# Kernel tuning notes

Hardware: AMD Instinct MI355X
Metric: run time of the kernel (lower is better)

The kernel has to match this reference:

```python
import jax, jax.numpy as jnp
import numpy as np

B, S, D, H = 16, 8192, 512, 512
NEG_INF = -1e18


def setup_inputs() -> dict:
    key0 = jax.random.key(0)
    ks = jax.random.split(key0, 8)
    scale = 1.0 / np.sqrt(D)
    return {
        "query": jax.random.normal(ks[0], (B, D), dtype=jnp.float32),
        "key": jax.random.normal(ks[1], (B, S, D), dtype=jnp.float32),
        "mask": jax.random.bernoulli(ks[2], 0.1, (B, S)),
        # q_proj: Linear(D -> H) with bias
        "Wq": jax.random.uniform(ks[3], (H, D), jnp.float32, -scale, scale),
        "bq": jax.random.uniform(ks[4], (H,), jnp.float32, -scale, scale),
        # k_proj: Conv1d(D -> H, kernel=1) == pointwise Linear with bias
        "Wk": jax.random.uniform(ks[5], (H, D), jnp.float32, -scale, scale),
        "bk": jax.random.uniform(ks[6], (H,), jnp.float32, -scale, scale),
        # out_proj: Linear(H -> 1, bias=False), init uniform(-1, 1)
        "w_out": jax.random.uniform(ks[7], (H,), jnp.float32, -1.0, 1.0),
    }


def reference(query, key, mask, Wq, bq, Wk, bk, w_out):
    # q_proj: (B, D) -> (B, H)
    q_h = query @ Wq.T + bq
    # k_proj (1x1 conv): (B, S, D) -> (B, S, H)
    k_h = jnp.einsum("bsd,hd->bsh", key, Wk) + bk
    # score = w_out . (q_h broadcast + k_h)  -> (B, S)
    attn_weight = jnp.einsum("bsh,h->bs", q_h[:, None, :] + k_h, w_out)
    attn_weight = jnp.where(mask, NEG_INF, attn_weight)
    attn_prob = jax.nn.softmax(attn_weight, axis=-1)
    # weighted sum over projected keys: (B, H)
    attn = jnp.einsum("bsh,bs->bh", k_h, attn_prob)
    return attn, attn_weight
```

## Files before the change

kernel.cpp:

```cpp
#include <hip/hip_runtime.h>
#include <math.h>

#define BB 16
#define SS 8192
#define DD 512
#define HH 512
#define NEG_INF (-1e18f)
#define BPB 64

__device__ __forceinline__ float dot8(float4 a0, float4 a1, float4 b0, float4 b1) {
  return a0.x*b0.x + a0.y*b0.y + a0.z*b0.z + a0.w*b0.w
       + a1.x*b1.x + a1.y*b1.y + a1.z*b1.z + a1.w*b1.w;
}

template <int CTRL>
__device__ __forceinline__ float dpp_add0(float x) {
  return x + __int_as_float(__builtin_amdgcn_update_dpp(
      0, __float_as_int(x), CTRL, 0xf, 0xf, true));
}
__device__ __forceinline__ float wave_red_sum(float x) {
  x = dpp_add0<0x111>(x);
  x = dpp_add0<0x112>(x);
  x = dpp_add0<0x114>(x);
  x = dpp_add0<0x118>(x);
  x = dpp_add0<0x142>(x);
  x = dpp_add0<0x143>(x);
  return x;
}
__device__ __forceinline__ float lane63(float x) {
  return __int_as_float(__builtin_amdgcn_readlane(__float_as_int(x), 63));
}
template <int CTRL>
__device__ __forceinline__ float dpp_maxstep(float x) {
  int y = __builtin_amdgcn_update_dpp(
      __float_as_int(x), __float_as_int(x), CTRL, 0xf, 0xf, false);
  return fmaxf(x, __int_as_float(y));
}
__device__ __forceinline__ float wave_red_max(float x) {
  x = dpp_maxstep<0x111>(x); x = dpp_maxstep<0x112>(x);
  x = dpp_maxstep<0x114>(x); x = dpp_maxstep<0x118>(x);
  x = dpp_maxstep<0x142>(x); x = dpp_maxstep<0x143>(x);
  return x;
}

__global__ __launch_bounds__(256) void k_prep(
    const float* __restrict__ Wq, const float* __restrict__ Wk,
    const float* __restrict__ wout, const float* __restrict__ bq,
    const float* __restrict__ bk, float* __restrict__ v,
    float* __restrict__ w2, float* __restrict__ c0)
{
  int blk = blockIdx.x;
  int t = threadIdx.x;
  if (blk == 128) {
    if (t < 64) {
      float part = 0.f;
      #pragma unroll
      for (int i = 0; i < 8; ++i) {
        int h = t + 64 * i;
        part += wout[h] * (bq[h] + bk[h]);
      }
      part = wave_red_sum(part);
      if (t == 63) c0[0] = part;
    }
    return;
  }
  int j = blk & 63;
  const float* W = (blk < 64) ? Wk : Wq;
  float* outp = (blk < 64) ? v : w2;
  int dsl = j * 8;
  int h0 = t, h1 = t + 256;
  const float4* r0 = (const float4*)(W + (size_t)h0 * DD + dsl);
  const float4* r1 = (const float4*)(W + (size_t)h1 * DD + dsl);
  float4 a0 = r0[0], a1 = r0[1], b0 = r1[0], b1 = r1[1];
  float wA = wout[h0], wB = wout[h1];
  float acc[8];
  acc[0] = wA*a0.x + wB*b0.x; acc[1] = wA*a0.y + wB*b0.y;
  acc[2] = wA*a0.z + wB*b0.z; acc[3] = wA*a0.w + wB*b0.w;
  acc[4] = wA*a1.x + wB*b1.x; acc[5] = wA*a1.y + wB*b1.y;
  acc[6] = wA*a1.z + wB*b1.z; acc[7] = wA*a1.w + wB*b1.w;
  __shared__ float red[256][9];
  #pragma unroll
  for (int k = 0; k < 8; ++k) red[t][k] = acc[k];
  __syncthreads();
  for (int st = 128; st; st >>= 1) {
    if (t < st) {
      #pragma unroll
      for (int k = 0; k < 8; ++k) red[t][k] += red[t + st][k];
    }
    __syncthreads();
  }
  if (t < 8) outp[dsl + t] = red[0][t];
}

__global__ __launch_bounds__(256, 4) void k_score(
    const float* __restrict__ key, const int* __restrict__ mask,
    const float* __restrict__ query, const float* __restrict__ ws_v,
    const float* __restrict__ ws_w2, const float* __restrict__ ws_c0,
    float* __restrict__ scores, float* __restrict__ partials)
{
  int blk = blockIdx.x;
  int b = blk / BPB;
  int pb = blk % BPB;
  const int rows = SS / BPB;
  int s0 = pb * rows;
  int wave = threadIdx.x >> 6;
  int lane = threadIdx.x & 63;

  const float4* vv = (const float4*)ws_v;
  float4 v0 = vv[lane], v1 = vv[64 + lane];

  float qc;
  {
    const float4* q4 = (const float4*)(query + (size_t)b * DD);
    const float4* w24 = (const float4*)ws_w2;
    float qp = wave_red_sum(dot8(q4[lane], q4[64 + lane], w24[lane], w24[64 + lane]));
    qc = lane63(qp) + ws_c0[0];
  }

  const float4* keyb = (const float4*)(key + (size_t)b * SS * DD);
  const int* maskb = mask + b * SS;

  float m = -INFINITY, l = 0.f;
  float4 u0 = {0.f,0.f,0.f,0.f}, u1 = {0.f,0.f,0.f,0.f};

  const int nit = rows / 16;
  int s = s0 + wave * 4;

  float4 r0a, r0b, r1a, r1b, r2a, r2b, r3a, r3b;
  {
    const float4* p0 = keyb + (size_t)s * (DD / 4);
    r0a = p0[lane];       r0b = p0[64 + lane];
    r1a = p0[128 + lane]; r1b = p0[192 + lane];
    r2a = p0[256 + lane]; r2b = p0[320 + lane];
    r3a = p0[384 + lane]; r3b = p0[448 + lane];
  }
  int4 mk = *(const int4*)(maskb + s);

  for (int i = 0; i < nit; ++i) {
    float4 n0a=r0a, n0b=r0b, n1a=r1a, n1b=r1b, n2a=r2a, n2b=r2b, n3a=r3a, n3b=r3b;
    int4 nmk = {0,0,0,0};
    if (i + 1 < nit) {
      const float4* p0 = keyb + (size_t)(s + 16) * (DD / 4);
      n0a = p0[lane];       n0b = p0[64 + lane];
      n1a = p0[128 + lane]; n1b = p0[192 + lane];
      n2a = p0[256 + lane]; n2b = p0[320 + lane];
      n3a = p0[384 + lane]; n3b = p0[448 + lane];
      nmk = *(const int4*)(maskb + s + 16);
    }
    float p0v = wave_red_sum(dot8(r0a, r0b, v0, v1));
    float p1v = wave_red_sum(dot8(r1a, r1b, v0, v1));
    float p2v = wave_red_sum(dot8(r2a, r2b, v0, v1));
    float p3v = wave_red_sum(dot8(r3a, r3b, v0, v1));
    float d0 = lane63(p0v), d1 = lane63(p1v);
    float d2 = lane63(p2v), d3 = lane63(p3v);
    float sc0 = mk.x ? NEG_INF : (d0 + qc);
    float sc1 = mk.y ? NEG_INF : (d1 + qc);
    float sc2 = mk.z ? NEG_INF : (d2 + qc);
    float sc3 = mk.w ? NEG_INF : (d3 + qc);
    if (lane == 0) {
      float4 st = {sc0, sc1, sc2, sc3};
      *(float4*)(scores + (size_t)b * SS + s) = st;
    }
    float mn = fmaxf(fmaxf(fmaxf(sc0, sc1), fmaxf(sc2, sc3)), m);
    if (mn > m) {
      float sc = __expf(m - mn);
      l *= sc;
      u0.x *= sc; u0.y *= sc; u0.z *= sc; u0.w *= sc;
      u1.x *= sc; u1.y *= sc; u1.z *= sc; u1.w *= sc;
      m = mn;
    }
    float e0 = __expf(sc0 - m), e1 = __expf(sc1 - m);
    float e2 = __expf(sc2 - m), e3 = __expf(sc3 - m);
    l += (e0 + e1) + (e2 + e3);
    u0.x += e0*r0a.x + e1*r1a.x + e2*r2a.x + e3*r3a.x;
    u0.y += e0*r0a.y + e1*r1a.y + e2*r2a.y + e3*r3a.y;
    u0.z += e0*r0a.z + e1*r1a.z + e2*r2a.z + e3*r3a.z;
    u0.w += e0*r0a.w + e1*r1a.w + e2*r2a.w + e3*r3a.w;
    u1.x += e0*r0b.x + e1*r1b.x + e2*r2b.x + e3*r3b.x;
    u1.y += e0*r0b.y + e1*r1b.y + e2*r2b.y + e3*r3b.y;
    u1.z += e0*r0b.z + e1*r1b.z + e2*r2b.z + e3*r3b.z;
    u1.w += e0*r0b.w + e1*r1b.w + e2*r2b.w + e3*r3b.w;
    r0a=n0a; r0b=n0b; r1a=n1a; r1b=n1b; r2a=n2a; r2b=n2b; r3a=n3a; r3b=n3b;
    mk = nmk; s += 16;
  }

  __shared__ float ls_m[4], ls_l[4];
  __shared__ __align__(16) float ls_u[4][DD];
  ls_u[wave][4 * lane + 0] = u0.x; ls_u[wave][4 * lane + 1] = u0.y;
  ls_u[wave][4 * lane + 2] = u0.z; ls_u[wave][4 * lane + 3] = u0.w;
  ls_u[wave][256 + 4 * lane + 0] = u1.x; ls_u[wave][256 + 4 * lane + 1] = u1.y;
  ls_u[wave][256 + 4 * lane + 2] = u1.z; ls_u[wave][256 + 4 * lane + 3] = u1.w;
  if (lane == 0) { ls_m[wave] = m; ls_l[wave] = l; }
  __syncthreads();

  float M = fmaxf(fmaxf(ls_m[0], ls_m[1]), fmaxf(ls_m[2], ls_m[3]));
  float f0 = __expf(ls_m[0] - M), f1 = __expf(ls_m[1] - M);
  float f2 = __expf(ls_m[2] - M), f3 = __expf(ls_m[3] - M);
  int d = threadIdx.x;
  float ua = ls_u[0][d] * f0 + ls_u[1][d] * f1 + ls_u[2][d] * f2 + ls_u[3][d] * f3;
  float ub = ls_u[0][d + 256] * f0 + ls_u[1][d + 256] * f1
           + ls_u[2][d + 256] * f2 + ls_u[3][d + 256] * f3;
  float* part = partials + (size_t)(b * BPB + pb) * (DD + 2);
  part[2 + d] = ua;
  part[2 + 256 + d] = ub;
  if (threadIdx.x == 0) {
    part[0] = M;
    part[1] = ls_l[0] * f0 + ls_l[1] * f1 + ls_l[2] * f2 + ls_l[3] * f3;
  }
}

__global__ __launch_bounds__(256) void k_out(
    const float* __restrict__ Wk, const float* __restrict__ bk,
    const float* __restrict__ partials, float* __restrict__ attn)
{
  int b = blockIdx.x >> 4;
  int hc = blockIdx.x & 15;
  int tid = threadIdx.x;
  int wave = tid >> 6, lane = tid & 63;
  __shared__ __align__(16) float ubar[DD];
  __shared__ float fsh[BPB];
  __shared__ float dsh;
  const float* pbase = partials + (size_t)b * BPB * (DD + 2);

  if (tid < 64) {
    float mp = pbase[tid * (DD + 2)];
    float lp = pbase[tid * (DD + 2) + 1];
    float M = lane63(wave_red_max(mp));
    float f = __expf(mp - M);
    fsh[tid] = f;
    float dn = wave_red_sum(lp * f);
    if (tid == 63) dsh = dn;
  }
  __syncthreads();

  float inv = 1.f / dsh;
  float ua = 0.f, ub_ = 0.f;
  #pragma unroll 8
  for (int p = 0; p < BPB; ++p) {
    float f = fsh[p];
    ua  += pbase[p * (DD + 2) + 2 + tid] * f;
    ub_ += pbase[p * (DD + 2) + 2 + 256 + tid] * f;
  }
  ubar[tid] = ua * inv;
  ubar[tid + 256] = ub_ * inv;
  __syncthreads();

  const float4* ub4 = (const float4*)ubar;
  float4 x0 = ub4[lane], x1 = ub4[64 + lane];
  #pragma unroll
  for (int j = 0; j < 8; ++j) {
    int h = hc * 32 + wave * 8 + j;
    const float4* wr = (const float4*)(Wk + (size_t)h * DD);
    float p = wave_red_sum(dot8(wr[lane], wr[64 + lane], x0, x1));
    if (lane == 63) attn[b * HH + h] = p + bk[h];
  }
}

extern "C" void kernel_launch(void* const* d_in, const int* in_sizes, int n_in,
                              void* d_out, int out_size, void* d_ws, size_t ws_size,
                              hipStream_t stream) {
  const float* query = (const float*)d_in[0];
  const float* key   = (const float*)d_in[1];
  const int*   mask  = (const int*)d_in[2];
  const float* Wq    = (const float*)d_in[3];
  const float* bq    = (const float*)d_in[4];
  const float* Wk    = (const float*)d_in[5];
  const float* bk    = (const float*)d_in[6];
  const float* wout  = (const float*)d_in[7];

  float* out    = (float*)d_out;
  float* attn   = out;
  float* scores = out + BB * HH;
  float* ws     = (float*)d_ws;

  float* ws_v  = ws;
  float* ws_w2 = ws + 512;
  float* ws_c0 = ws + 1024;
  float* partials = ws + 1040;

  k_prep<<<dim3(129), dim3(256), 0, stream>>>(Wq, Wk, wout, bq, bk,
                                              ws_v, ws_w2, ws_c0);
  k_score<<<dim3(BB * BPB), dim3(256), 0, stream>>>(key, mask, query, ws_v,
                                                    ws_w2, ws_c0, scores, partials);
  k_out<<<dim3(BB * 16), dim3(256), 0, stream>>>(Wk, bk, partials, attn);
}
```

Before: 60.97 us.

## Fuse output reduction into score kernel via last-block atomic counter

```diff
diff --git a/kernel.cpp b/kernel.cpp
--- a/kernel.cpp
+++ b/kernel.cpp
@@ -47,11 +47,13 @@
     const float* __restrict__ Wq, const float* __restrict__ Wk,
     const float* __restrict__ wout, const float* __restrict__ bq,
     const float* __restrict__ bk, float* __restrict__ v,
-    float* __restrict__ w2, float* __restrict__ c0)
+    float* __restrict__ w2, float* __restrict__ c0,
+    unsigned* __restrict__ cnt)
 {
   int blk = blockIdx.x;
   int t = threadIdx.x;
   if (blk == 128) {
+    if (t < BB) cnt[t] = 0u;
     if (t < 64) {
       float part = 0.f;
       #pragma unroll
@@ -96,7 +98,9 @@
     const float* __restrict__ key, const int* __restrict__ mask,
     const float* __restrict__ query, const float* __restrict__ ws_v,
     const float* __restrict__ ws_w2, const float* __restrict__ ws_c0,
-    float* __restrict__ scores, float* __restrict__ partials)
+    const float* __restrict__ Wk, const float* __restrict__ bk,
+    float* __restrict__ scores, float* __restrict__ partials,
+    unsigned* __restrict__ cnt, float* __restrict__ attn)
 {
   int blk = blockIdx.x;
   int b = blk / BPB;
@@ -105,6 +109,10 @@
   int s0 = pb * rows;
   int wave = threadIdx.x >> 6;
   int lane = threadIdx.x & 63;
+
+  __shared__ __align__(16) float smem[4 * DD];
+  __shared__ float ls_m[4], ls_l[4], dsh;
+  __shared__ unsigned sh_old;
 
   const float4* vv = (const float4*)ws_v;
   float4 v0 = vv[lane], v1 = vv[64 + lane];
@@ -184,12 +192,10 @@
     mk = nmk; s += 16;
   }
 
-  __shared__ float ls_m[4], ls_l[4];
-  __shared__ __align__(16) float ls_u[4][DD];
-  ls_u[wave][4 * lane + 0] = u0.x; ls_u[wave][4 * lane + 1] = u0.y;
-  ls_u[wave][4 * lane + 2] = u0.z; ls_u[wave][4 * lane + 3] = u0.w;
-  ls_u[wave][256 + 4 * lane + 0] = u1.x; ls_u[wave][256 + 4 * lane + 1] = u1.y;
-  ls_u[wave][256 + 4 * lane + 2] = u1.z; ls_u[wave][256 + 4 * lane + 3] = u1.w;
+  smem[wave * DD + 4 * lane + 0] = u0.x; smem[wave * DD + 4 * lane + 1] = u0.y;
+  smem[wave * DD + 4 * lane + 2] = u0.z; smem[wave * DD + 4 * lane + 3] = u0.w;
+  smem[wave * DD + 256 + 4 * lane + 0] = u1.x; smem[wave * DD + 256 + 4 * lane + 1] = u1.y;
+  smem[wave * DD + 256 + 4 * lane + 2] = u1.z; smem[wave * DD + 256 + 4 * lane + 3] = u1.w;
   if (lane == 0) { ls_m[wave] = m; ls_l[wave] = l; }
   __syncthreads();
 
@@ -197,9 +203,10 @@
   float f0 = __expf(ls_m[0] - M), f1 = __expf(ls_m[1] - M);
   float f2 = __expf(ls_m[2] - M), f3 = __expf(ls_m[3] - M);
   int d = threadIdx.x;
-  float ua = ls_u[0][d] * f0 + ls_u[1][d] * f1 + ls_u[2][d] * f2 + ls_u[3][d] * f3;
-  float ub = ls_u[0][d + 256] * f0 + ls_u[1][d + 256] * f1
-           + ls_u[2][d + 256] * f2 + ls_u[3][d + 256] * f3;
+  float ua = smem[d] * f0 + smem[DD + d] * f1
+           + smem[2 * DD + d] * f2 + smem[3 * DD + d] * f3;
+  float ub = smem[d + 256] * f0 + smem[DD + d + 256] * f1
+           + smem[2 * DD + d + 256] * f2 + smem[3 * DD + d + 256] * f3;
   float* part = partials + (size_t)(b * BPB + pb) * (DD + 2);
   part[2 + d] = ua;
   part[2 + 256 + d] = ub;
@@ -207,26 +214,26 @@
     part[0] = M;
     part[1] = ls_l[0] * f0 + ls_l[1] * f1 + ls_l[2] * f2 + ls_l[3] * f3;
   }
-}
-
-__global__ __launch_bounds__(256) void k_out(
-    const float* __restrict__ Wk, const float* __restrict__ bk,
-    const float* __restrict__ partials, float* __restrict__ attn)
-{
-  int b = blockIdx.x >> 4;
-  int hc = blockIdx.x & 15;
+
+  __syncthreads();
+  if (threadIdx.x == 0) {
+    __threadfence();
+    sh_old = atomicAdd(&cnt[b], 1u);
+  }
+  __syncthreads();
+  if (sh_old != BPB - 1) return;
+
+  __threadfence();
+  float* ubar = smem;
+  float* fsh  = smem + DD;
+  const float* pbase = partials + (size_t)b * BPB * (DD + 2);
   int tid = threadIdx.x;
-  int wave = tid >> 6, lane = tid & 63;
-  __shared__ __align__(16) float ubar[DD];
-  __shared__ float fsh[BPB];
-  __shared__ float dsh;
-  const float* pbase = partials + (size_t)b * BPB * (DD + 2);
 
   if (tid < 64) {
     float mp = pbase[tid * (DD + 2)];
     float lp = pbase[tid * (DD + 2) + 1];
-    float M = lane63(wave_red_max(mp));
-    float f = __expf(mp - M);
+    float Mx = lane63(wave_red_max(mp));
+    float f = __expf(mp - Mx);
     fsh[tid] = f;
     float dn = wave_red_sum(lp * f);
     if (tid == 63) dsh = dn;
@@ -234,22 +241,22 @@
   __syncthreads();
 
   float inv = 1.f / dsh;
-  float ua = 0.f, ub_ = 0.f;
+  float sa = 0.f, sb = 0.f;
   #pragma unroll 8
   for (int p = 0; p < BPB; ++p) {
     float f = fsh[p];
-    ua  += pbase[p * (DD + 2) + 2 + tid] * f;
-    ub_ += pbase[p * (DD + 2) + 2 + 256 + tid] * f;
-  }
-  ubar[tid] = ua * inv;
-  ubar[tid + 256] = ub_ * inv;
+    sa += pbase[p * (DD + 2) + 2 + tid] * f;
+    sb += pbase[p * (DD + 2) + 2 + 256 + tid] * f;
+  }
+  ubar[tid] = sa * inv;
+  ubar[tid + 256] = sb * inv;
   __syncthreads();
 
   const float4* ub4 = (const float4*)ubar;
   float4 x0 = ub4[lane], x1 = ub4[64 + lane];
-  #pragma unroll
-  for (int j = 0; j < 8; ++j) {
-    int h = hc * 32 + wave * 8 + j;
+  #pragma unroll 4
+  for (int j = 0; j < 128; ++j) {
+    int h = wave * 128 + j;
     const float4* wr = (const float4*)(Wk + (size_t)h * DD);
     float p = wave_red_sum(dot8(wr[lane], wr[64 + lane], x0, x1));
     if (lane == 63) attn[b * HH + h] = p + bk[h];
@@ -276,11 +283,12 @@
   float* ws_v  = ws;
   float* ws_w2 = ws + 512;
   float* ws_c0 = ws + 1024;
-  float* partials = ws + 1040;
+  unsigned* cnt = (unsigned*)(ws + 1040);
+  float* partials = ws + 1056;
 
   k_prep<<<dim3(129), dim3(256), 0, stream>>>(Wq, Wk, wout, bq, bk,
-                                              ws_v, ws_w2, ws_c0);
+                                              ws_v, ws_w2, ws_c0, cnt);
   k_score<<<dim3(BB * BPB), dim3(256), 0, stream>>>(key, mask, query, ws_v,
-                                                    ws_w2, ws_c0, scores, partials);
-  k_out<<<dim3(BB * 16), dim3(256), 0, stream>>>(Wk, bk, partials, attn);
-}
+                                                    ws_w2, ws_c0, Wk, bk,
+                                                    scores, partials, cnt, attn);
+}
```

Result: slower. 162.8 us (+167.1%).

## Template split count, use 128 blocks per batch with 2 rows per wave

Applied to the files above, without the earlier changes.

```diff
diff --git a/kernel.cpp b/kernel.cpp
--- a/kernel.cpp
+++ b/kernel.cpp
@@ -6,7 +6,6 @@
 #define DD 512
 #define HH 512
 #define NEG_INF (-1e18f)
-#define BPB 64
 
 __device__ __forceinline__ float dot8(float4 a0, float4 a1, float4 b0, float4 b1) {
   return a0.x*b0.x + a0.y*b0.y + a0.z*b0.z + a0.w*b0.w
@@ -92,16 +91,17 @@
   if (t < 8) outp[dsl + t] = red[0][t];
 }
 
-__global__ __launch_bounds__(256, 4) void k_score(
+template <int NPB>
+__global__ __launch_bounds__(256, 6) void k_score(
     const float* __restrict__ key, const int* __restrict__ mask,
     const float* __restrict__ query, const float* __restrict__ ws_v,
     const float* __restrict__ ws_w2, const float* __restrict__ ws_c0,
     float* __restrict__ scores, float* __restrict__ partials)
 {
   int blk = blockIdx.x;
-  int b = blk / BPB;
-  int pb = blk % BPB;
-  const int rows = SS / BPB;
+  int b = blk / NPB;
+  int pb = blk % NPB;
+  const int rows = SS / NPB;
   int s0 = pb * rows;
   int wave = threadIdx.x >> 6;
   int lane = threadIdx.x & 63;
@@ -123,45 +123,36 @@
   float m = -INFINITY, l = 0.f;
   float4 u0 = {0.f,0.f,0.f,0.f}, u1 = {0.f,0.f,0.f,0.f};
 
-  const int nit = rows / 16;
-  int s = s0 + wave * 4;
-
-  float4 r0a, r0b, r1a, r1b, r2a, r2b, r3a, r3b;
+  const int nit = rows / 8;
+  int s = s0 + wave * 2;
+
+  float4 r0a, r0b, r1a, r1b;
   {
     const float4* p0 = keyb + (size_t)s * (DD / 4);
     r0a = p0[lane];       r0b = p0[64 + lane];
     r1a = p0[128 + lane]; r1b = p0[192 + lane];
-    r2a = p0[256 + lane]; r2b = p0[320 + lane];
-    r3a = p0[384 + lane]; r3b = p0[448 + lane];
-  }
-  int4 mk = *(const int4*)(maskb + s);
+  }
+  int2 mk = *(const int2*)(maskb + s);
 
   for (int i = 0; i < nit; ++i) {
-    float4 n0a=r0a, n0b=r0b, n1a=r1a, n1b=r1b, n2a=r2a, n2b=r2b, n3a=r3a, n3b=r3b;
-    int4 nmk = {0,0,0,0};
+    float4 n0a=r0a, n0b=r0b, n1a=r1a, n1b=r1b;
+    int2 nmk = {0,0};
     if (i + 1 < nit) {
-      const float4* p0 = keyb + (size_t)(s + 16) * (DD / 4);
+      const float4* p0 = keyb + (size_t)(s + 8) * (DD / 4);
       n0a = p0[lane];       n0b = p0[64 + lane];
       n1a = p0[128 + lane]; n1b = p0[192 + lane];
-      n2a = p0[256 + lane]; n2b = p0[320 + lane];
-      n3a = p0[384 + lane]; n3b = p0[448 + lane];
-      nmk = *(const int4*)(maskb + s + 16);
+      nmk = *(const int2*)(maskb + s + 8);
     }
     float p0v = wave_red_sum(dot8(r0a, r0b, v0, v1));
     float p1v = wave_red_sum(dot8(r1a, r1b, v0, v1));
-    float p2v = wave_red_sum(dot8(r2a, r2b, v0, v1));
-    float p3v = wave_red_sum(dot8(r3a, r3b, v0, v1));
     float d0 = lane63(p0v), d1 = lane63(p1v);
-    float d2 = lane63(p2v), d3 = lane63(p3v);
     float sc0 = mk.x ? NEG_INF : (d0 + qc);
     float sc1 = mk.y ? NEG_INF : (d1 + qc);
-    float sc2 = mk.z ? NEG_INF : (d2 + qc);
-    float sc3 = mk.w ? NEG_INF : (d3 + qc);
     if (lane == 0) {
-      float4 st = {sc0, sc1, sc2, sc3};
-      *(float4*)(scores + (size_t)b * SS + s) = st;
-    }
-    float mn = fmaxf(fmaxf(fmaxf(sc0, sc1), fmaxf(sc2, sc3)), m);
+      float2 st = {sc0, sc1};
+      *(float2*)(scores + (size_t)b * SS + s) = st;
+    }
+    float mn = fmaxf(fmaxf(sc0, sc1), m);
     if (mn > m) {
       float sc = __expf(m - mn);
       l *= sc;
@@ -170,18 +161,13 @@
       m = mn;
     }
     float e0 = __expf(sc0 - m), e1 = __expf(sc1 - m);
-    float e2 = __expf(sc2 - m), e3 = __expf(sc3 - m);
-    l += (e0 + e1) + (e2 + e3);
-    u0.x += e0*r0a.x + e1*r1a.x + e2*r2a.x + e3*r3a.x;
-    u0.y += e0*r0a.y + e1*r1a.y + e2*r2a.y + e3*r3a.y;
-    u0.z += e0*r0a.z + e1*r1a.z + e2*r2a.z + e3*r3a.z;
-    u0.w += e0*r0a.w + e1*r1a.w + e2*r2a.w + e3*r3a.w;
-    u1.x += e0*r0b.x + e1*r1b.x + e2*r2b.x + e3*r3b.x;
-    u1.y += e0*r0b.y + e1*r1b.y + e2*r2b.y + e3*r3b.y;
-    u1.z += e0*r0b.z + e1*r1b.z + e2*r2b.z + e3*r3b.z;
-    u1.w += e0*r0b.w + e1*r1b.w + e2*r2b.w + e3*r3b.w;
-    r0a=n0a; r0b=n0b; r1a=n1a; r1b=n1b; r2a=n2a; r2b=n2b; r3a=n3a; r3b=n3b;
-    mk = nmk; s += 16;
+    l += e0 + e1;
+    u0.x += e0*r0a.x + e1*r1a.x; u0.y += e0*r0a.y + e1*r1a.y;
+    u0.z += e0*r0a.z + e1*r1a.z; u0.w += e0*r0a.w + e1*r1a.w;
+    u1.x += e0*r0b.x + e1*r1b.x; u1.y += e0*r0b.y + e1*r1b.y;
+    u1.z += e0*r0b.z + e1*r1b.z; u1.w += e0*r0b.w + e1*r1b.w;
+    r0a=n0a; r0b=n0b; r1a=n1a; r1b=n1b;
+    mk = nmk; s += 8;
   }
 
   __shared__ float ls_m[4], ls_l[4];
@@ -200,7 +186,7 @@
   float ua = ls_u[0][d] * f0 + ls_u[1][d] * f1 + ls_u[2][d] * f2 + ls_u[3][d] * f3;
   float ub = ls_u[0][d + 256] * f0 + ls_u[1][d + 256] * f1
            + ls_u[2][d + 256] * f2 + ls_u[3][d + 256] * f3;
-  float* part = partials + (size_t)(b * BPB + pb) * (DD + 2);
+  float* part = partials + (size_t)(b * NPB + pb) * (DD + 2);
   part[2 + d] = ua;
   part[2 + 256 + d] = ub;
   if (threadIdx.x == 0) {
@@ -209,6 +195,7 @@
   }
 }
 
+template <int NPB>
 __global__ __launch_bounds__(256) void k_out(
     const float* __restrict__ Wk, const float* __restrict__ bk,
     const float* __restrict__ partials, float* __restrict__ attn)
@@ -218,25 +205,37 @@
   int tid = threadIdx.x;
   int wave = tid >> 6, lane = tid & 63;
   __shared__ __align__(16) float ubar[DD];
-  __shared__ float fsh[BPB];
+  __shared__ float fsh[NPB];
   __shared__ float dsh;
-  const float* pbase = partials + (size_t)b * BPB * (DD + 2);
+  const float* pbase = partials + (size_t)b * NPB * (DD + 2);
 
   if (tid < 64) {
-    float mp = pbase[tid * (DD + 2)];
-    float lp = pbase[tid * (DD + 2) + 1];
-    float M = lane63(wave_red_max(mp));
-    float f = __expf(mp - M);
-    fsh[tid] = f;
-    float dn = wave_red_sum(lp * f);
-    if (tid == 63) dsh = dn;
+    if (NPB == 128) {
+      float mp0 = pbase[tid * (DD + 2)];
+      float mp1 = pbase[(tid + 64) * (DD + 2)];
+      float lp0 = pbase[tid * (DD + 2) + 1];
+      float lp1 = pbase[(tid + 64) * (DD + 2) + 1];
+      float M = lane63(wave_red_max(fmaxf(mp0, mp1)));
+      float f0 = __expf(mp0 - M), f1 = __expf(mp1 - M);
+      fsh[tid] = f0; fsh[tid + 64] = f1;
+      float dn = wave_red_sum(lp0 * f0 + lp1 * f1);
+      if (tid == 63) dsh = dn;
+    } else {
+      float mp = pbase[tid * (DD + 2)];
+      float lp = pbase[tid * (DD + 2) + 1];
+      float M = lane63(wave_red_max(mp));
+      float f = __expf(mp - M);
+      fsh[tid] = f;
+      float dn = wave_red_sum(lp * f);
+      if (tid == 63) dsh = dn;
+    }
   }
   __syncthreads();
 
   float inv = 1.f / dsh;
   float ua = 0.f, ub_ = 0.f;
   #pragma unroll 8
-  for (int p = 0; p < BPB; ++p) {
+  for (int p = 0; p < NPB; ++p) {
     float f = fsh[p];
     ua  += pbase[p * (DD + 2) + 2 + tid] * f;
     ub_ += pbase[p * (DD + 2) + 2 + 256 + tid] * f;
@@ -280,7 +279,15 @@
 
   k_prep<<<dim3(129), dim3(256), 0, stream>>>(Wq, Wk, wout, bq, bk,
                                               ws_v, ws_w2, ws_c0);
-  k_score<<<dim3(BB * BPB), dim3(256), 0, stream>>>(key, mask, query, ws_v,
-                                                    ws_w2, ws_c0, scores, partials);
-  k_out<<<dim3(BB * 16), dim3(256), 0, stream>>>(Wk, bk, partials, attn);
-}
+
+  size_t need128 = (1040 + (size_t)BB * 128 * (DD + 2)) * sizeof(float);
+  if (ws_size >= need128) {
+    k_score<128><<<dim3(BB * 128), dim3(256), 0, stream>>>(
+        key, mask, query, ws_v, ws_w2, ws_c0, scores, partials);
+    k_out<128><<<dim3(BB * 16), dim3(256), 0, stream>>>(Wk, bk, partials, attn);
+  } else {
+    k_score<64><<<dim3(BB * 64), dim3(256), 0, stream>>>(
+        key, mask, query, ws_v, ws_w2, ws_c0, scores, partials);
+    k_out<64><<<dim3(BB * 16), dim3(256), 0, stream>>>(Wk, bk, partials, attn);
+  }
+}
```

Measured after the change: 63.25 us. 1.04x slower.
